# Kernel optimization log

Hardware: AMD Instinct MI355X
Metric: run time of the kernel (lower is better)

## Reference

```python
import jax, jax.numpy as jnp
import numpy as np

B, S, D, H, DH = 4, 2048, 512, 8, 64  # batch, seq, input_dim, heads, per-head output_dim


def setup_inputs() -> dict:
    key = jax.random.key(0)
    ks = jax.random.split(key, 10)
    scale = 0.02
    inp = {
        "x": jax.random.normal(ks[0], (B, S, D), dtype=jnp.float32),
        "biological_mask": jnp.ones((B, S), dtype=bool),
        "Wq": jax.random.normal(ks[1], (D, H * DH), dtype=jnp.float32) * scale,
        "bq": jnp.zeros((H * DH,), dtype=jnp.float32),
        "Wk": jax.random.normal(ks[2], (D, H * DH), dtype=jnp.float32) * scale,
        "bk": jnp.zeros((H * DH,), dtype=jnp.float32),
        "Wv": jax.random.normal(ks[3], (D, H * DH), dtype=jnp.float32) * scale,
        "bv": jnp.zeros((H * DH,), dtype=jnp.float32),
        "Wo": jax.random.normal(ks[4], (H * DH, DH), dtype=jnp.float32) * scale,
        "bo": jnp.zeros((DH,), dtype=jnp.float32),
        "prior_weight": jnp.full((1,), 0.1, dtype=jnp.float32),
    }
    return inp


def reference(x, biological_mask, Wq, bq, Wk, bk, Wv, bv, Wo, bo, prior_weight):
    b, s, _ = x.shape
    inv_sqrt_dh = jnp.float32(1.0 / np.sqrt(DH))
    # projections -> [B,H,S,DH]
    q = (x @ Wq + bq).reshape(b, s, H, DH).transpose(0, 2, 1, 3)
    k = (x @ Wk + bk).reshape(b, s, H, DH).transpose(0, 2, 1, 3)
    v = (x @ Wv + bv).reshape(b, s, H, DH).transpose(0, 2, 1, 3)
    # scores [B,H,S,S]
    scores = jnp.einsum("bhqd,bhkd->bhqk", q, k) * inv_sqrt_dh
    # biological prior: identity matrix, broadcast over batch and heads
    prior = jnp.eye(s, dtype=scores.dtype)[None, None, :, :]
    scores = scores + prior_weight[0] * prior
    attn = jax.nn.softmax(scores, axis=-1)  # dropout is identity in eval mode
    attended = jnp.einsum("bhqk,bhkd->bhqd", attn, v)
    attended = attended.transpose(0, 2, 1, 3).reshape(b, s, H * DH)
    return attended @ Wo + bo
```

## Files before the change

kernel.cpp:

```cpp
#include <hip/hip_runtime.h>
#include <hip/hip_bf16.h>

#define B_ 4
#define S_ 2048
#define D_ 512
#define H_ 8
#define DH_ 64
#define HD_ 512
#define M_ 8192
#define QKVN 1536
#define QKN 1024
#define LOG2E 1.4426950408889634f

typedef __attribute__((ext_vector_type(8))) short bf16x8;
typedef __attribute__((ext_vector_type(4))) float f32x4;
typedef unsigned short u16;

__device__ inline u16 f2bf(float f) {
    __hip_bfloat16 h = __float2bfloat16(f);
    return *reinterpret_cast<u16*>(&h);
}

__device__ inline void async_cp16(const void* g, void* l) {
    __builtin_amdgcn_global_load_lds(
        (const __attribute__((address_space(1))) unsigned int*)g,
        (__attribute__((address_space(3))) unsigned int*)l, 16, 0, 0);
}

__global__ __launch_bounds__(256) void castbf(const float* __restrict__ src,
                                              u16* __restrict__ dst, int n8)
{
    int i = blockIdx.x * 256 + threadIdx.x;
    if (i < n8) {
        float4 a = *reinterpret_cast<const float4*>(&src[(size_t)i * 8]);
        float4 b = *reinterpret_cast<const float4*>(&src[(size_t)i * 8 + 4]);
        bf16x8 o;
        o[0] = f2bf(a.x); o[1] = f2bf(a.y); o[2] = f2bf(a.z); o[3] = f2bf(a.w);
        o[4] = f2bf(b.x); o[5] = f2bf(b.y); o[6] = f2bf(b.z); o[7] = f2bf(b.w);
        *reinterpret_cast<bf16x8*>(&dst[(size_t)i * 8]) = o;
    }
}

__global__ __launch_bounds__(256) void wprep(
    const float* __restrict__ Wq, const float* __restrict__ Wk,
    const float* __restrict__ Wv, const float* __restrict__ Wo,
    u16* __restrict__ WqkvT, u16* __restrict__ WoT)
{
    const int z = blockIdx.z;
    const float* src; u16* dst; int R, C;
    if (z < 3) { src = (z == 0) ? Wq : (z == 1) ? Wk : Wv;
                 dst = WqkvT + (size_t)z * 512 * 512; R = 512; C = 512; }
    else       { if (blockIdx.x) return; src = Wo; dst = WoT; R = 512; C = 64; }

    __shared__ u16 T[64][65];
    const int tid = threadIdx.x;
    const int c0 = blockIdx.x * 64, r0 = blockIdx.y * 64;
#pragma unroll
    for (int i = 0; i < 4; ++i) {
        int idx = i * 256 + tid;
        int r = idx >> 4, q4 = (idx & 15) << 2;
        float4 vv = *reinterpret_cast<const float4*>(&src[(size_t)(r0 + r) * C + c0 + q4]);
        T[r][q4 + 0] = f2bf(vv.x); T[r][q4 + 1] = f2bf(vv.y);
        T[r][q4 + 2] = f2bf(vv.z); T[r][q4 + 3] = f2bf(vv.w);
    }
    __syncthreads();
#pragma unroll
    for (int i = 0; i < 2; ++i) {
        int idx = i * 256 + tid;
        int cc = idx >> 3, jj = idx & 7;
        bf16x8 o;
#pragma unroll
        for (int e = 0; e < 8; ++e) o[e] = (short)T[jj * 8 + e][cc];
        *reinterpret_cast<bf16x8*>(&dst[(size_t)(c0 + cc) * R + r0 + jj * 8]) = o;
    }
}

__global__ __launch_bounds__(256) void gemm_qkv(
    const u16* __restrict__ A, const u16* __restrict__ BT,
    const float* __restrict__ bq, const float* __restrict__ bk,
    const float* __restrict__ bv, u16* __restrict__ qk,
    u16* __restrict__ vT, float qscale)
{
    __shared__ __align__(16) u16 As[128 * 64];
    __shared__ __align__(16) u16 Bs[128 * 64];
    const int tid = threadIdx.x, lane = tid & 63, w = tid >> 6;
    const int l15 = lane & 15, l4 = lane >> 4;
    const int tm = blockIdx.y * 128, tn = blockIdx.x * 128;
    const int wm = (w >> 1) * 64, wn = (w & 1) * 64;

    f32x4 acc[4][4] = {};

    for (int k0 = 0; k0 < 512; k0 += 64) {
#pragma unroll
        for (int i = 0; i < 4; ++i) {
            int call = w * 4 + i;
            int c = call * 64 + lane;
            int r = c >> 3, j = c & 7;
            async_cp16(A + (size_t)(tm + r) * 512 + k0 + ((j ^ (r & 7)) << 3),
                       &As[call * 512]);
            async_cp16(BT + (size_t)(tn + r) * 512 + k0 + ((j ^ (r & 7)) << 3),
                       &Bs[call * 512]);
        }
        __syncthreads();
#pragma unroll
        for (int ks = 0; ks < 2; ++ks) {
            bf16x8 af[4], bf[4];
#pragma unroll
            for (int mf = 0; mf < 4; ++mf) {
                int r = wm + mf * 16 + l15;
                int j = ks * 4 + l4;
                af[mf] = *reinterpret_cast<const bf16x8*>(&As[(r * 8 + (j ^ (r & 7))) * 8]);
            }
#pragma unroll
            for (int nf = 0; nf < 4; ++nf) {
                int r = wn + nf * 16 + l15;
                int j = ks * 4 + l4;
                bf[nf] = *reinterpret_cast<const bf16x8*>(&Bs[(r * 8 + (j ^ (r & 7))) * 8]);
            }
#pragma unroll
            for (int mf = 0; mf < 4; ++mf)
#pragma unroll
                for (int nf = 0; nf < 4; ++nf)
                    acc[mf][nf] = __builtin_amdgcn_mfma_f32_16x16x32_bf16(
                        af[mf], bf[nf], acc[mf][nf], 0, 0, 0);
        }
        __syncthreads();
    }
#pragma unroll
    for (int nf = 0; nf < 4; ++nf) {
        const int col = tn + wn + nf * 16 + l15;
        if (col < QKN) {
            const float bias_v = (col < 512) ? bq[col] : bk[col - 512];
            const float scl = (col < 512) ? qscale : 1.0f;
#pragma unroll
            for (int mf = 0; mf < 4; ++mf)
#pragma unroll
                for (int r = 0; r < 4; ++r) {
                    int row = tm + wm + mf * 16 + l4 * 4 + r;
                    qk[(size_t)row * QKN + col] = f2bf((acc[mf][nf][r] + bias_v) * scl);
                }
        } else {
            const int dcol = col - QKN;
            const float bias_v = bv[dcol];
            const int hh = dcol >> 6, dd = dcol & 63;
#pragma unroll
            for (int mf = 0; mf < 4; ++mf) {
                int row0 = tm + wm + mf * 16 + l4 * 4;
                int bb = row0 >> 11, s0 = row0 & 2047;
                ushort4 pk;
                pk.x = f2bf(acc[mf][nf][0] + bias_v);
                pk.y = f2bf(acc[mf][nf][1] + bias_v);
                pk.z = f2bf(acc[mf][nf][2] + bias_v);
                pk.w = f2bf(acc[mf][nf][3] + bias_v);
                *reinterpret_cast<ushort4*>(
                    &vT[((size_t)(bb * 8 + hh) * 64 + dd) * S_ + s0]) = pk;
            }
        }
    }
}

__global__ __launch_bounds__(256, 4) void flash_mfma(
    const u16* __restrict__ qk, const u16* __restrict__ vT,
    const float* __restrict__ pw_ptr, u16* __restrict__ att)
{
    __shared__ __align__(16) u16 Kb[2][4096];
    __shared__ __align__(16) u16 Vb[2][4096];

    const int tid = threadIdx.x, lane = tid & 63, w = tid >> 6;
    const int l15 = lane & 15, l4 = lane >> 4;
    const int bid = blockIdx.x;
    const int x = bid & 7, g = bid >> 3;
    const int bh = x * 4 + (g >> 5), qt = g & 31;
    const int h = bh & 7, b = bh >> 3;
    const float pwl = pw_ptr[0] * LOG2E;

    const u16* qbase = qk + (size_t)b * S_ * QKN + h * 64;
    const u16* kbase = qbase + 512;
    const u16* vtb   = vT + (size_t)bh * DH_ * S_;

    const int qrow0 = qt * 64 + w * 16;
    bf16x8 qb[2];
#pragma unroll
    for (int ks2 = 0; ks2 < 2; ++ks2)
        qb[ks2] = *reinterpret_cast<const bf16x8*>(
            &qbase[(size_t)(qrow0 + l15) * QKN + ks2 * 32 + l4 * 8]);

    f32x4 accv[4] = {};
    float l_r = 0.f;
    const int diag_t = qt;

#define STAGE(buf, jj) do {                                                        \
    _Pragma("unroll")                                                              \
    for (int i_ = 0; i_ < 2; ++i_) {                                               \
        int call_ = w * 2 + i_;                                                    \
        int c_ = call_ * 64 + lane;                                                \
        int rho_ = c_ >> 3, j_ = c_ & 7;                                           \
        int pi_ = (rho_ & 32) | ((rho_ & 12) << 1) | ((rho_ & 16) >> 2)            \
                | (rho_ & 3);                                                      \
        async_cp16(kbase + (size_t)((jj) + pi_) * QKN + ((j_ ^ (rho_ & 7)) << 3),  \
                   &Kb[buf][call_ * 512]);                                         \
        async_cp16(vtb + (size_t)rho_ * S_ + (jj) + ((j_ ^ (rho_ & 7)) << 3),      \
                   &Vb[buf][call_ * 512]);                                         \
    } } while (0)

    STAGE(0, 0);
    __syncthreads();
    int cur = 0;

    for (int t = 0; t < 32; ++t) {
        const int j0 = t << 6;
        if (t < 31) STAGE(cur ^ 1, j0 + 64);

        f32x4 s[4] = {};
        __builtin_amdgcn_s_setprio(1);
#pragma unroll
        for (int c = 0; c < 4; ++c)
#pragma unroll
            for (int ks2 = 0; ks2 < 2; ++ks2) {
                const int rr = c * 16 + l15;
                const int sl = ks2 * 4 + l4;
                bf16x8 ka = *reinterpret_cast<const bf16x8*>(
                    &Kb[cur][(rr * 8 + (sl ^ (rr & 7))) * 8]);
                s[c] = __builtin_amdgcn_mfma_f32_16x16x32_bf16(ka, qb[ks2], s[c], 0, 0, 0);
            }
        __builtin_amdgcn_s_setprio(0);

        if (t == diag_t) {
#pragma unroll
            for (int c = 0; c < 4; ++c)
#pragma unroll
                for (int r = 0; r < 4; ++r) {
                    int kv = (c >> 1) * 32 + l4 * 8 + (c & 1) * 4 + r;
                    if (j0 + kv == qrow0 + l15) s[c][r] += pwl;
                }
        }

        bf16x8 pa[2];
#pragma unroll
        for (int ks = 0; ks < 2; ++ks)
#pragma unroll
            for (int d2 = 0; d2 < 2; ++d2)
#pragma unroll
                for (int r = 0; r < 4; ++r) {
                    float p = exp2f(s[ks * 2 + d2][r]);
                    l_r += p;
                    pa[ks][d2 * 4 + r] = (short)f2bf(p);
                }

        __builtin_amdgcn_s_setprio(1);
#pragma unroll
        for (int nf = 0; nf < 4; ++nf) {
            const int d = nf * 16 + l15;
#pragma unroll
            for (int ks = 0; ks < 2; ++ks) {
                const int sl = ks * 4 + l4;
                bf16x8 vb = *reinterpret_cast<const bf16x8*>(
                    &Vb[cur][(d * 8 + (sl ^ (d & 7))) * 8]);
                accv[nf] = __builtin_amdgcn_mfma_f32_16x16x32_bf16(pa[ks], vb, accv[nf], 0, 0, 0);
            }
        }
        __builtin_amdgcn_s_setprio(0);

        __syncthreads();
        cur ^= 1;
    }
#undef STAGE

    float lt = l_r;
    lt += __shfl_xor(lt, 16);
    lt += __shfl_xor(lt, 32);
#pragma unroll
    for (int r = 0; r < 4; ++r) {
        float inv = 1.0f / __shfl(lt, l4 * 4 + r);
        int row = qrow0 + l4 * 4 + r;
#pragma unroll
        for (int nf = 0; nf < 4; ++nf)
            att[(size_t)(b * S_ + row) * HD_ + h * 64 + nf * 16 + l15] =
                f2bf(accv[nf][r] * inv);
    }
}

__global__ __launch_bounds__(64) void out_proj(
    const u16* __restrict__ att, const u16* __restrict__ WoT,
    const float* __restrict__ bo, float* __restrict__ out)
{
    const int lane = threadIdx.x;
    const int l15 = lane & 15, l4 = lane >> 4;
    const int row0 = blockIdx.x * 16;

    f32x4 acc[4] = {};
#pragma unroll 4
    for (int ks = 0; ks < 16; ++ks) {
        bf16x8 a = *reinterpret_cast<const bf16x8*>(
            &att[(size_t)(row0 + l15) * 512 + ks * 32 + l4 * 8]);
#pragma unroll
        for (int nf = 0; nf < 4; ++nf) {
            bf16x8 bb = *reinterpret_cast<const bf16x8*>(
                &WoT[(size_t)(nf * 16 + l15) * 512 + ks * 32 + l4 * 8]);
            acc[nf] = __builtin_amdgcn_mfma_f32_16x16x32_bf16(a, bb, acc[nf], 0, 0, 0);
        }
    }
#pragma unroll
    for (int nf = 0; nf < 4; ++nf) {
        int n = nf * 16 + l15;
        float bias_v = bo[n];
#pragma unroll
        for (int r = 0; r < 4; ++r)
            out[(size_t)(row0 + l4 * 4 + r) * 64 + n] = acc[nf][r] + bias_v;
    }
}

extern "C" void kernel_launch(void* const* d_in, const int* in_sizes, int n_in,
                              void* d_out, int out_size, void* d_ws, size_t ws_size,
                              hipStream_t stream)
{
    const float* x  = (const float*)d_in[0];
    const float* Wq = (const float*)d_in[2];
    const float* bq = (const float*)d_in[3];
    const float* Wk = (const float*)d_in[4];
    const float* bk = (const float*)d_in[5];
    const float* Wv = (const float*)d_in[6];
    const float* bv = (const float*)d_in[7];
    const float* Wo = (const float*)d_in[8];
    const float* bo = (const float*)d_in[9];
    const float* pw = (const float*)d_in[10];

    u16* ws = (u16*)d_ws;
    size_t o = 0;
    u16* xb    = ws + o; o += (size_t)M_ * D_;
    u16* WqkvT = ws + o; o += (size_t)QKVN * D_;
    u16* WoT   = ws + o; o += (size_t)DH_ * HD_;
    u16* qkb   = ws + o; o += (size_t)M_ * QKN;
    u16* vTt   = ws + o; o += (size_t)M_ * HD_;
    u16* att   = ws + o; o += (size_t)M_ * HD_;

    dim3 blk(256);
    castbf<<<dim3(M_ * D_ / 8 / 256), blk, 0, stream>>>(x, xb, M_ * D_ / 8);
    wprep<<<dim3(8, 8, 4), blk, 0, stream>>>(Wq, Wk, Wv, Wo, WqkvT, WoT);

    gemm_qkv<<<dim3(QKVN / 128, M_ / 128), blk, 0, stream>>>(
        xb, WqkvT, bq, bk, bv, qkb, vTt, 0.125f * LOG2E);

    flash_mfma<<<dim3(1024), blk, 0, stream>>>(qkb, vTt, pw, att);

    out_proj<<<dim3(M_ / 16), dim3(64), 0, stream>>>(att, WoT, bo, (float*)d_out);
}
```

Baseline: 107.9 us.

## Double per-wave query rows in flash kernel and compute row sums via MFMA

Each wave now processes 32 query rows (two 16-row fragments), so a block covers 128 queries and the grid shrinks from 1024 to 512 blocks. Each K/V tile loaded into LDS is reused across twice as many queries, which halves K/V staging traffic and LDS reads per query. The softmax denominator is now accumulated by an MFMA against a vector of bf16 ones instead of scalar adds plus shuffles. In exchange, register pressure rises, the occupancy hint in launch bounds is dropped, and bf16-rounded probabilities are summed, which changes numerics slightly.

```diff
diff --git a/kernel.cpp b/kernel.cpp
--- a/kernel.cpp
+++ b/kernel.cpp
@@ -159,7 +159,7 @@
     }
 }
 
-__global__ __launch_bounds__(256, 4) void flash_mfma(
+__global__ __launch_bounds__(256) void flash_mfma(
     const u16* __restrict__ qk, const u16* __restrict__ vT,
     const float* __restrict__ pw_ptr, u16* __restrict__ att)
 {
@@ -170,7 +170,7 @@
     const int l15 = lane & 15, l4 = lane >> 4;
     const int bid = blockIdx.x;
     const int x = bid & 7, g = bid >> 3;
-    const int bh = x * 4 + (g >> 5), qt = g & 31;
+    const int bh = x * 4 + (g >> 4), qt = g & 15;
     const int h = bh & 7, b = bh >> 3;
     const float pwl = pw_ptr[0] * LOG2E;
 
@@ -178,16 +178,21 @@
     const u16* kbase = qbase + 512;
     const u16* vtb   = vT + (size_t)bh * DH_ * S_;
 
-    const int qrow0 = qt * 64 + w * 16;
-    bf16x8 qb[2];
-#pragma unroll
-    for (int ks2 = 0; ks2 < 2; ++ks2)
-        qb[ks2] = *reinterpret_cast<const bf16x8*>(
-            &qbase[(size_t)(qrow0 + l15) * QKN + ks2 * 32 + l4 * 8]);
-
-    f32x4 accv[4] = {};
-    float l_r = 0.f;
-    const int diag_t = qt;
+    const int qrow0 = qt * 128 + w * 32;
+    bf16x8 qb[2][2];
+#pragma unroll
+    for (int nf = 0; nf < 2; ++nf)
+#pragma unroll
+        for (int ks = 0; ks < 2; ++ks)
+            qb[nf][ks] = *reinterpret_cast<const bf16x8*>(
+                &qbase[(size_t)(qrow0 + nf * 16 + l15) * QKN + ks * 32 + l4 * 8]);
+
+    const bf16x8 ones = {(short)0x3F80, (short)0x3F80, (short)0x3F80, (short)0x3F80,
+                         (short)0x3F80, (short)0x3F80, (short)0x3F80, (short)0x3F80};
+
+    f32x4 accv[2][4] = {};
+    f32x4 accl[2] = {};
+    const int diag_t = qrow0 >> 6;
 
 #define STAGE(buf, jj) do {                                                        \
     _Pragma("unroll")                                                              \
@@ -211,17 +216,18 @@
         const int j0 = t << 6;
         if (t < 31) STAGE(cur ^ 1, j0 + 64);
 
-        f32x4 s[4] = {};
+        f32x4 s[4][2] = {};
         __builtin_amdgcn_s_setprio(1);
 #pragma unroll
         for (int c = 0; c < 4; ++c)
 #pragma unroll
-            for (int ks2 = 0; ks2 < 2; ++ks2) {
+            for (int ks = 0; ks < 2; ++ks) {
                 const int rr = c * 16 + l15;
-                const int sl = ks2 * 4 + l4;
+                const int sl = ks * 4 + l4;
                 bf16x8 ka = *reinterpret_cast<const bf16x8*>(
                     &Kb[cur][(rr * 8 + (sl ^ (rr & 7))) * 8]);
-                s[c] = __builtin_amdgcn_mfma_f32_16x16x32_bf16(ka, qb[ks2], s[c], 0, 0, 0);
+                s[c][0] = __builtin_amdgcn_mfma_f32_16x16x32_bf16(ka, qb[0][ks], s[c][0], 0, 0, 0);
+                s[c][1] = __builtin_amdgcn_mfma_f32_16x16x32_bf16(ka, qb[1][ks], s[c][1], 0, 0, 0);
             }
         __builtin_amdgcn_s_setprio(0);
 
@@ -229,34 +235,42 @@
 #pragma unroll
             for (int c = 0; c < 4; ++c)
 #pragma unroll
-                for (int r = 0; r < 4; ++r) {
-                    int kv = (c >> 1) * 32 + l4 * 8 + (c & 1) * 4 + r;
-                    if (j0 + kv == qrow0 + l15) s[c][r] += pwl;
-                }
-        }
-
-        bf16x8 pa[2];
-#pragma unroll
-        for (int ks = 0; ks < 2; ++ks)
-#pragma unroll
-            for (int d2 = 0; d2 < 2; ++d2)
-#pragma unroll
-                for (int r = 0; r < 4; ++r) {
-                    float p = exp2f(s[ks * 2 + d2][r]);
-                    l_r += p;
-                    pa[ks][d2 * 4 + r] = (short)f2bf(p);
-                }
+                for (int nf = 0; nf < 2; ++nf)
+#pragma unroll
+                    for (int r = 0; r < 4; ++r) {
+                        int kv = (c >> 1) * 32 + l4 * 8 + (c & 1) * 4 + r;
+                        if (j0 + kv == qrow0 + nf * 16 + l15) s[c][nf][r] += pwl;
+                    }
+        }
+
+        bf16x8 pa[2][2];
+#pragma unroll
+        for (int nf = 0; nf < 2; ++nf)
+#pragma unroll
+            for (int ks = 0; ks < 2; ++ks)
+#pragma unroll
+                for (int d2 = 0; d2 < 2; ++d2)
+#pragma unroll
+                    for (int r = 0; r < 4; ++r)
+                        pa[nf][ks][d2 * 4 + r] =
+                            (short)f2bf(exp2f(s[ks * 2 + d2][nf][r]));
 
         __builtin_amdgcn_s_setprio(1);
 #pragma unroll
-        for (int nf = 0; nf < 4; ++nf) {
-            const int d = nf * 16 + l15;
+        for (int ks = 0; ks < 2; ++ks) {
+            accl[0] = __builtin_amdgcn_mfma_f32_16x16x32_bf16(pa[0][ks], ones, accl[0], 0, 0, 0);
+            accl[1] = __builtin_amdgcn_mfma_f32_16x16x32_bf16(pa[1][ks], ones, accl[1], 0, 0, 0);
+        }
+#pragma unroll
+        for (int n = 0; n < 4; ++n) {
+            const int d = n * 16 + l15;
 #pragma unroll
             for (int ks = 0; ks < 2; ++ks) {
                 const int sl = ks * 4 + l4;
                 bf16x8 vb = *reinterpret_cast<const bf16x8*>(
                     &Vb[cur][(d * 8 + (sl ^ (d & 7))) * 8]);
-                accv[nf] = __builtin_amdgcn_mfma_f32_16x16x32_bf16(pa[ks], vb, accv[nf], 0, 0, 0);
+                accv[0][n] = __builtin_amdgcn_mfma_f32_16x16x32_bf16(pa[0][ks], vb, accv[0][n], 0, 0, 0);
+                accv[1][n] = __builtin_amdgcn_mfma_f32_16x16x32_bf16(pa[1][ks], vb, accv[1][n], 0, 0, 0);
             }
         }
         __builtin_amdgcn_s_setprio(0);
@@ -266,18 +280,17 @@
     }
 #undef STAGE
 
-    float lt = l_r;
-    lt += __shfl_xor(lt, 16);
-    lt += __shfl_xor(lt, 32);
-#pragma unroll
-    for (int r = 0; r < 4; ++r) {
-        float inv = 1.0f / __shfl(lt, l4 * 4 + r);
-        int row = qrow0 + l4 * 4 + r;
-#pragma unroll
-        for (int nf = 0; nf < 4; ++nf)
-            att[(size_t)(b * S_ + row) * HD_ + h * 64 + nf * 16 + l15] =
-                f2bf(accv[nf][r] * inv);
-    }
+#pragma unroll
+    for (int nf = 0; nf < 2; ++nf)
+#pragma unroll
+        for (int r = 0; r < 4; ++r) {
+            float inv = 1.0f / accl[nf][r];
+            int row = qrow0 + nf * 16 + l4 * 4 + r;
+#pragma unroll
+            for (int n = 0; n < 4; ++n)
+                att[(size_t)(b * S_ + row) * HD_ + h * 64 + n * 16 + l15] =
+                    f2bf(accv[nf][n][r] * inv);
+        }
 }
 
 __global__ __launch_bounds__(64) void out_proj(
@@ -341,7 +354,7 @@
     gemm_qkv<<<dim3(QKVN / 128, M_ / 128), blk, 0, stream>>>(
         xb, WqkvT, bq, bk, bv, qkb, vTt, 0.125f * LOG2E);
 
-    flash_mfma<<<dim3(1024), blk, 0, stream>>>(qkb, vTt, pw, att);
+    flash_mfma<<<dim3(512), blk, 0, stream>>>(qkb, vTt, pw, att);
 
     out_proj<<<dim3(M_ / 16), dim3(64), 0, stream>>>(att, WoT, bo, (float*)d_out);
 }
```

Result: slower. 113.9 us (+5.5%).
